# Kernel tuning notes

Measured on AMD Instinct MI355X. Metric: run time of the kernel, lower is better.

The kernel has to match this reference:

```python
import jax, jax.numpy as jnp
import numpy as np
import math

B, S, D, H = 4, 2048, 1024, 16
HD = D // H  # head_dim = 64


def _rope_tables(max_len, half_dim, theta=10000.0):
    inv_freq = 1.0 / (theta ** (jnp.arange(0, half_dim, dtype=jnp.float32) / half_dim))
    ang = jnp.arange(max_len, dtype=jnp.float32)[:, None] * inv_freq[None, :]  # [max_len, half_dim]
    return jnp.cos(ang), jnp.sin(ang)


def _apply_rope(x, cos, sin):
    # x: [B, H, S, HD]; cos/sin: [S, HD/2]
    x1, x2 = x[..., ::2], x[..., 1::2]
    # matches torch.cat([x1*cos - x2*sin, x1*sin + x2*cos], dim=-1)
    return jnp.concatenate([x1 * cos - x2 * sin, x1 * sin + x2 * cos], axis=-1)


def setup_inputs() -> dict:
    key = jax.random.key(0)
    kx, kq, ko = jax.random.split(key, 3)
    x = jax.random.normal(kx, (B, S, D), dtype=jnp.float32)
    Wqkv = jax.random.normal(kq, (D, 3 * D), dtype=jnp.float32) / math.sqrt(D)
    Wout = jax.random.normal(ko, (D, D), dtype=jnp.float32) / math.sqrt(D)
    cos, sin = _rope_tables(S, HD // 2)
    # causal additive mask, per-batch as in module signature [B, S, S]
    causal = jnp.where(jnp.tril(jnp.ones((S, S), dtype=bool)), 0.0, -1e9).astype(jnp.float32)
    mask = jnp.broadcast_to(causal, (B, S, S))
    return {"x": x, "cos": cos, "sin": sin, "mask": mask, "Wqkv": Wqkv, "Wout": Wout}


def reference(x, cos, sin, mask, Wqkv, Wout):
    b, s, d = x.shape
    qkv = x @ Wqkv  # [B, S, 3D]
    q, k, v = jnp.split(qkv, 3, axis=-1)
    def to_heads(t):
        return t.reshape(b, s, H, HD).transpose(0, 2, 1, 3)  # [B, H, S, HD]
    q, k, v = to_heads(q), to_heads(k), to_heads(v)
    q = _apply_rope(q, cos[:s], sin[:s])
    k = _apply_rope(k, cos[:s], sin[:s])
    scores = jnp.einsum("bhqd,bhkd->bhqk", q, k) / math.sqrt(HD)
    attn = jax.nn.softmax(scores + mask[:, None, :, :], axis=-1)
    out = jnp.einsum("bhqk,bhkd->bhqd", attn, v)  # [B, H, S, HD]
    out = out.transpose(0, 2, 1, 3).reshape(b, s, d)
    return out @ Wout
```

## Files before the change

### kernel.cpp

```cpp
#include <hip/hip_runtime.h>
#include <hip/hip_bf16.h>
#include <stdint.h>

#define B_   4
#define S_   2048
#define D_   1024
#define H_   16
#define HD_  64
#define BH_  (B_*H_)
#define MROWS (B_*S_)

typedef short  short8  __attribute__((ext_vector_type(8)));
typedef float  floatx4 __attribute__((ext_vector_type(4)));

__device__ __forceinline__ ushort f2bf(float f) {
    union { float f; uint32_t u; } v; v.f = f;
    uint32_t u = v.u;
    return (ushort)((u + 0x7FFFu + ((u >> 16) & 1u)) >> 16);
}
__device__ __forceinline__ float u2f(uint32_t u) {
    union { uint32_t u; float f; } v; v.u = u; return v.f;
}
__device__ __forceinline__ uint32_t f2u(float f) {
    union { float f; uint32_t u; } v; v.f = f; return v.u;
}

__device__ __forceinline__ void gl_lds16(const ushort* g, ushort* l) {
    __builtin_amdgcn_global_load_lds(
        (const __attribute__((address_space(1))) unsigned int*)g,
        (__attribute__((address_space(3))) unsigned int*)l,
        16, 0, 0);
}

__global__ __launch_bounds__(256)
void k_prep(const float* __restrict__ x, const float* __restrict__ Wqkv,
            const float* __restrict__ Wout,
            ushort* __restrict__ Xbf, ushort* __restrict__ WqkvT, ushort* __restrict__ WoutT) {
    __shared__ float tile[32][33];
    int blk = blockIdx.x;
    int tid = threadIdx.x;
    if (blk >= 4096) {
        int i = (blk - 4096) * 1024 + tid * 4;
        float4 f = *(const float4*)(x + i);
        ushort4 o; o.x = f2bf(f.x); o.y = f2bf(f.y); o.z = f2bf(f.z); o.w = f2bf(f.w);
        *(ushort4*)(Xbf + i) = o;
        return;
    }
    const float* in; ushort* out; int R, C, bx, by;
    if (blk < 3072) { in = Wqkv; out = WqkvT; R = D_; C = 3 * D_; bx = (blk % 96) * 32; by = (blk / 96) * 32; }
    else            { int b2 = blk - 3072; in = Wout; out = WoutT; R = D_; C = D_; bx = (b2 % 32) * 32; by = (b2 / 32) * 32; }
    int tx = tid & 31, ty = tid >> 5;
    #pragma unroll
    for (int j = 0; j < 32; j += 8)
        tile[ty + j][tx] = in[(size_t)(by + ty + j) * C + bx + tx];
    __syncthreads();
    #pragma unroll
    for (int j = 0; j < 32; j += 8)
        out[(size_t)(bx + ty + j) * R + by + tx] = f2bf(tile[tx][ty + j]);
}

#define BM 128
#define BN 128
#define BK 64

template<int EPI>
__global__ __launch_bounds__(256)
void k_gemm(const ushort* __restrict__ A, const ushort* __restrict__ Bt,
            float* __restrict__ outF,
            ushort* __restrict__ q_out, ushort* __restrict__ k_out, ushort* __restrict__ v_out,
            int M, int N, int K) {
    __shared__ __align__(16) ushort As[BM * 64];
    __shared__ __align__(16) ushort Bs[BN * 64];
    int tid  = threadIdx.x;
    int lane = tid & 63;
    int wave = tid >> 6;
    int quad = lane >> 4;
    int l16  = lane & 15;
    int bm = blockIdx.y * BM;
    int bn = blockIdx.x * BN;
    int wm = (wave >> 1) * 64;
    int wn = (wave & 1) * 64;

    floatx4 acc[4][4] = {};

    for (int k0 = 0; k0 < K; k0 += BK) {
        __syncthreads();
        #pragma unroll
        for (int i = 0; i < 4; i++) {
            int c   = i * 256 + tid;
            int row = c >> 3;
            int gc  = (c & 7) ^ (row & 7);
            gl_lds16(&A[(size_t)(bm + row) * K + k0 + gc * 8],  &As[c * 8]);
            gl_lds16(&Bt[(size_t)(bn + row) * K + k0 + gc * 8], &Bs[c * 8]);
        }
        __syncthreads();
        #pragma unroll
        for (int kk = 0; kk < 2; kk++) {
            short8 af[4], bf[4];
            #pragma unroll
            for (int mt = 0; mt < 4; mt++)
                af[mt] = *(const short8*)&As[(wm + mt * 16 + l16) * 64 +
                                             (((kk * 4 + quad) ^ (l16 & 7)) << 3)];
            #pragma unroll
            for (int nt = 0; nt < 4; nt++)
                bf[nt] = *(const short8*)&Bs[(wn + nt * 16 + l16) * 64 +
                                             (((kk * 4 + quad) ^ (l16 & 7)) << 3)];
            #pragma unroll
            for (int mt = 0; mt < 4; mt++)
                #pragma unroll
                for (int nt = 0; nt < 4; nt++)
                    acc[mt][nt] = __builtin_amdgcn_mfma_f32_16x16x32_bf16(af[mt], bf[nt], acc[mt][nt], 0, 0, 0);
        }
    }

    #pragma unroll
    for (int mt = 0; mt < 4; mt++)
        #pragma unroll
        for (int nt = 0; nt < 4; nt++)
            #pragma unroll
            for (int r = 0; r < 4; r++) {
                int row = bm + wm + mt * 16 + quad * 4 + r;
                int col = bn + wn + nt * 16 + l16;
                float v = acc[mt][nt][r];
                if (EPI == 0) {
                    int which = col >> 10;
                    int rem   = col & 1023;
                    int h  = rem >> 6, hd = rem & 63;
                    int b  = row >> 11, s  = row & 2047;
                    size_t idx = ((size_t)(b * H_ + h) * S_ + s) * HD_ + hd;
                    ushort bv = f2bf(v);
                    ushort* dst = (which == 0) ? q_out : (which == 1) ? k_out : v_out;
                    dst[idx] = bv;
                } else {
                    outF[(size_t)row * N + col] = v;
                }
            }
}

__global__ __launch_bounds__(256)
void k_ropevt(ushort* __restrict__ Q, ushort* __restrict__ Kv,
              const ushort* __restrict__ Vb, ushort* __restrict__ VbT,
              const float* __restrict__ cosT, const float* __restrict__ sinT) {
    __shared__ __align__(16) ushort t[64 * 72];
    int blk = blockIdx.x;
    int tid = threadIdx.x;
    if (blk < 32768) {
        int wid  = (blk * 256 + tid) >> 6;
        int lane = tid & 63;
        int s  = wid & (S_ - 1);
        int bh = wid >> 11;
        int i  = lane & 31;
        float c  = cosT[s * 32 + i];
        float sn = sinT[s * 32 + i];
        size_t base = ((size_t)bh * S_ + s) * HD_;

        uint32_t uq = *(const uint32_t*)&Q[base + 2 * i];
        float x1 = u2f(uq << 16), x2 = u2f(uq & 0xFFFF0000u);
        float o  = (lane < 32) ? (x1 * c - x2 * sn) : (x1 * sn + x2 * c);
        Q[base + lane] = f2bf(o * 0.1803368801f);

        uint32_t uk = *(const uint32_t*)&Kv[base + 2 * i];
        x1 = u2f(uk << 16); x2 = u2f(uk & 0xFFFF0000u);
        o  = (lane < 32) ? (x1 * c - x2 * sn) : (x1 * sn + x2 * c);
        Kv[base + lane] = f2bf(o);
        return;
    }
    int b2 = blk - 32768;
    int bh = b2 >> 5;
    int s0 = (b2 & 31) * 64;
    int ss = tid >> 2, c0 = (tid & 3) * 16;
    size_t base = (size_t)bh * S_ * HD_;
    *(uint4*)&t[ss * 72 + c0]     = *(const uint4*)&Vb[base + (size_t)(s0 + ss) * HD_ + c0];
    *(uint4*)&t[ss * 72 + c0 + 8] = *(const uint4*)&Vb[base + (size_t)(s0 + ss) * HD_ + c0 + 8];
    __syncthreads();
    int hd = tid >> 2, q0 = (tid & 3) * 16;
    ushort tmp[16];
    #pragma unroll
    for (int e = 0; e < 16; e++) tmp[e] = t[(q0 + e) * 72 + hd];
    size_t obase = (size_t)bh * HD_ * S_ + (size_t)hd * S_ + s0 + q0;
    *(uint4*)&VbT[obase]     = *(const uint4*)&tmp[0];
    *(uint4*)&VbT[obase + 8] = *(const uint4*)&tmp[8];
}

__global__ __launch_bounds__(256, 4)
void k_attn(const ushort* __restrict__ Q, const ushort* __restrict__ K,
            const ushort* __restrict__ VT, ushort* __restrict__ O) {
    __shared__ __align__(16) ushort Ks[64 * 64];
    __shared__ __align__(16) ushort Vt[64 * 64];
    __shared__ __align__(16) ushort Pst[4][32 * 64];

    const int PI[16] = {15,14,11,10, 12,13,8,9, 2,3,6,7, 1,0,5,4};

    int tid  = threadIdx.x;
    int lane = tid & 63;
    int wave = tid >> 6;
    int quad = lane >> 4;
    int l16  = lane & 15;

    int bh   = blockIdx.x & 63;
    int qblk = PI[blockIdx.x >> 6];
    int qb0  = qblk * 128;
    size_t hbase = (size_t)bh * S_ * HD_;
    size_t vbase = (size_t)bh * HD_ * S_;

    int mrow[2] = { qb0 + wave * 16, qb0 + 64 + wave * 16 };

    short8 qf[2][2];
    #pragma unroll
    for (int m = 0; m < 2; m++)
        #pragma unroll
        for (int h = 0; h < 2; h++)
            qf[m][h] = *(const short8*)&Q[hbase + (size_t)(mrow[m] + l16) * HD_ + quad * 8 + h * 32];

    short8 ones;
    #pragma unroll
    for (int e = 0; e < 8; e++) ones[e] = (short)0x3F80;

    floatx4 acc[2][4] = {};
    floatx4 accl[2] = {};

    int c0r = tid >> 3;
    int c1r = (256 + tid) >> 3;
    const ushort* kp0 = &K[hbase + (size_t)c0r * HD_ + (((tid & 7) ^ (c0r & 7)) << 3)];
    const ushort* kp1 = &K[hbase + (size_t)c1r * HD_ + (((tid & 7) ^ (c1r & 7)) << 3)];
    const ushort* vp0 = &VT[vbase + (size_t)c0r * S_ + (((tid & 7) ^ (c0r & 7)) << 3)];
    const ushort* vp1 = &VT[vbase + (size_t)c1r * S_ + (((tid & 7) ^ (c1r & 7)) << 3)];

    int nk = 2 * qblk + 2;
    for (int kb = 0; kb < nk; kb++) {
        int k0 = kb * 64;
        __syncthreads();
        gl_lds16(kp0, &Ks[tid * 8]);
        gl_lds16(kp1, &Ks[(256 + tid) * 8]);
        gl_lds16(vp0, &Vt[tid * 8]);
        gl_lds16(vp1, &Vt[(256 + tid) * 8]);
        kp0 += 64 * HD_; kp1 += 64 * HD_; vp0 += 64; vp1 += 64;
        __syncthreads();

        bool act[2] = { k0 <= mrow[0] + 15, k0 <= mrow[1] + 15 };

        #pragma unroll
        for (int m = 0; m < 2; m++) {
            if (!act[m]) continue;
            floatx4 sc[4] = {};
            #pragma unroll
            for (int kt = 0; kt < 4; kt++)
                #pragma unroll
                for (int h = 0; h < 2; h++) {
                    short8 kf = *(const short8*)&Ks[(kt * 16 + l16) * 64 +
                                                    (((h * 4 + quad) ^ (l16 & 7)) << 3)];
                    sc[kt] = __builtin_amdgcn_mfma_f32_16x16x32_bf16(kf, qf[m][h], sc[kt], 0, 0, 0);
                }
            bool needMask = (k0 + 63 > mrow[m]);
            int qr = mrow[m] + l16;
            #pragma unroll
            for (int kt = 0; kt < 4; kt++) {
                float p[4];
                #pragma unroll
                for (int r = 0; r < 4; r++) {
                    float v = exp2f(sc[kt][r]);
                    if (needMask) {
                        int kc = k0 + kt * 16 + quad * 4 + r;
                        if (kc > qr) v = 0.0f;
                    }
                    p[r] = v;
                }
                uint2 pk;
                pk.x = __builtin_amdgcn_perm(f2u(p[1]) + 0x8000u, f2u(p[0]) + 0x8000u, 0x07060302u);
                pk.y = __builtin_amdgcn_perm(f2u(p[3]) + 0x8000u, f2u(p[2]) + 0x8000u, 0x07060302u);
                int pc = (kt * 4 + quad) ^ (l16 & 14);
                *(uint2*)&Pst[wave][(m * 16 + l16) * 64 + pc * 4] = pk;
            }
        }

        #pragma unroll
        for (int k2 = 0; k2 < 2; k2++) {
            short8 vb[4];
            #pragma unroll
            for (int nt = 0; nt < 4; nt++)
                vb[nt] = *(const short8*)&Vt[(nt * 16 + l16) * 64 +
                                             (((k2 * 4 + quad) ^ (l16 & 7)) << 3)];
            #pragma unroll
            for (int m = 0; m < 2; m++) {
                if (!act[m]) continue;
                int pe = (k2 * 8 + quad * 2) ^ (l16 & 14);
                short8 pa = *(const short8*)&Pst[wave][(m * 16 + l16) * 64 + pe * 4];
                #pragma unroll
                for (int nt = 0; nt < 4; nt++)
                    acc[m][nt] = __builtin_amdgcn_mfma_f32_16x16x32_bf16(pa, vb[nt], acc[m][nt], 0, 0, 0);
                accl[m] = __builtin_amdgcn_mfma_f32_16x16x32_bf16(pa, ones, accl[m], 0, 0, 0);
            }
        }
    }

    int b = bh >> 4, h = bh & 15;
    #pragma unroll
    for (int m = 0; m < 2; m++)
        #pragma unroll
        for (int r = 0; r < 4; r++) {
            float inv = 1.0f / accl[m][r];
            int qr = mrow[m] + quad * 4 + r;
            #pragma unroll
            for (int nt = 0; nt < 4; nt++)
                O[((size_t)(b * S_ + qr)) * D_ + h * HD_ + nt * 16 + l16] = f2bf(acc[m][nt][r] * inv);
        }
}

extern "C" void kernel_launch(void* const* d_in, const int* in_sizes, int n_in,
                              void* d_out, int out_size, void* d_ws, size_t ws_size,
                              hipStream_t stream) {
    const float* x    = (const float*)d_in[0];
    const float* cosT = (const float*)d_in[1];
    const float* sinT = (const float*)d_in[2];
    const float* Wqkv = (const float*)d_in[4];
    const float* Wout = (const float*)d_in[5];
    float* out = (float*)d_out;

    ushort* ws = (ushort*)d_ws;
    ushort* Xbf    = ws;
    ushort* WqkvT  = Xbf    + (size_t)MROWS * D_;
    ushort* WoutT  = WqkvT  + (size_t)3 * D_ * D_;
    ushort* Qb     = WoutT  + (size_t)D_ * D_;
    ushort* Kb     = Qb     + (size_t)BH_ * S_ * HD_;
    ushort* Vb     = Kb     + (size_t)BH_ * S_ * HD_;
    ushort* VbT    = Vb     + (size_t)BH_ * S_ * HD_;
    ushort* AO     = Xbf;

    k_prep<<<12288, 256, 0, stream>>>(x, Wqkv, Wout, Xbf, WqkvT, WoutT);
    k_gemm<0><<<dim3(3 * D_ / BN, MROWS / BM), 256, 0, stream>>>(Xbf, WqkvT, nullptr, Qb, Kb, Vb,
                                                                 MROWS, 3 * D_, D_);
    k_ropevt<<<34816, 256, 0, stream>>>(Qb, Kb, Vb, VbT, cosT, sinT);
    k_attn<<<1024, 256, 0, stream>>>(Qb, Kb, VbT, AO);
    k_gemm<1><<<dim3(D_ / BN, MROWS / BM), 256, 0, stream>>>(AO, WoutT, out, nullptr, nullptr, nullptr,
                                                             MROWS, D_, D_);
}
```

Baseline: 314.2 us.

## Split attention query block across eight waves and add MFMA priority hints

The attention kernel now runs 512 threads per block, with each of eight waves owning one 16-row query slice instead of four waves each owning two slices. Each thread loads half as much K/V per tile, and the P·V step moves inside the active-row branch. MFMA sections are wrapped in s_setprio, and the bf16 packing of P uses v_cvt_pk_bf16_f32 instead of manual rounding with perm. The intent is more wave-level parallelism and lower register pressure per wave, at the cost of more waves contending at each barrier.

```diff
diff --git a/kernel.cpp b/kernel.cpp
--- a/kernel.cpp
+++ b/kernel.cpp
@@ -182,12 +182,12 @@
     *(uint4*)&VbT[obase + 8] = *(const uint4*)&tmp[8];
 }
 
-__global__ __launch_bounds__(256, 4)
+__global__ __launch_bounds__(512, 8)
 void k_attn(const ushort* __restrict__ Q, const ushort* __restrict__ K,
             const ushort* __restrict__ VT, ushort* __restrict__ O) {
     __shared__ __align__(16) ushort Ks[64 * 64];
     __shared__ __align__(16) ushort Vt[64 * 64];
-    __shared__ __align__(16) ushort Pst[4][32 * 64];
+    __shared__ __align__(16) ushort Pst[8][16 * 64];
 
     const int PI[16] = {15,14,11,10, 12,13,8,9, 2,3,6,7, 1,0,5,4};
 
@@ -203,56 +203,49 @@
     size_t hbase = (size_t)bh * S_ * HD_;
     size_t vbase = (size_t)bh * HD_ * S_;
 
-    int mrow[2] = { qb0 + wave * 16, qb0 + 64 + wave * 16 };
-
-    short8 qf[2][2];
-    #pragma unroll
-    for (int m = 0; m < 2; m++)
-        #pragma unroll
-        for (int h = 0; h < 2; h++)
-            qf[m][h] = *(const short8*)&Q[hbase + (size_t)(mrow[m] + l16) * HD_ + quad * 8 + h * 32];
+    int mrow = qb0 + wave * 16;
+
+    short8 qf[2];
+    #pragma unroll
+    for (int h = 0; h < 2; h++)
+        qf[h] = *(const short8*)&Q[hbase + (size_t)(mrow + l16) * HD_ + quad * 8 + h * 32];
 
     short8 ones;
     #pragma unroll
     for (int e = 0; e < 8; e++) ones[e] = (short)0x3F80;
 
-    floatx4 acc[2][4] = {};
-    floatx4 accl[2] = {};
-
-    int c0r = tid >> 3;
-    int c1r = (256 + tid) >> 3;
-    const ushort* kp0 = &K[hbase + (size_t)c0r * HD_ + (((tid & 7) ^ (c0r & 7)) << 3)];
-    const ushort* kp1 = &K[hbase + (size_t)c1r * HD_ + (((tid & 7) ^ (c1r & 7)) << 3)];
-    const ushort* vp0 = &VT[vbase + (size_t)c0r * S_ + (((tid & 7) ^ (c0r & 7)) << 3)];
-    const ushort* vp1 = &VT[vbase + (size_t)c1r * S_ + (((tid & 7) ^ (c1r & 7)) << 3)];
+    floatx4 acc[4] = {};
+    floatx4 accl = {};
+
+    int srow = tid >> 3;
+    const ushort* kp = &K[hbase + (size_t)srow * HD_ + (((tid & 7) ^ (srow & 7)) << 3)];
+    const ushort* vp = &VT[vbase + (size_t)srow * S_ + (((tid & 7) ^ (srow & 7)) << 3)];
 
     int nk = 2 * qblk + 2;
     for (int kb = 0; kb < nk; kb++) {
         int k0 = kb * 64;
         __syncthreads();
-        gl_lds16(kp0, &Ks[tid * 8]);
-        gl_lds16(kp1, &Ks[(256 + tid) * 8]);
-        gl_lds16(vp0, &Vt[tid * 8]);
-        gl_lds16(vp1, &Vt[(256 + tid) * 8]);
-        kp0 += 64 * HD_; kp1 += 64 * HD_; vp0 += 64; vp1 += 64;
+        gl_lds16(kp, &Ks[tid * 8]);
+        gl_lds16(vp, &Vt[tid * 8]);
+        kp += 64 * HD_; vp += 64;
         __syncthreads();
 
-        bool act[2] = { k0 <= mrow[0] + 15, k0 <= mrow[1] + 15 };
-
-        #pragma unroll
-        for (int m = 0; m < 2; m++) {
-            if (!act[m]) continue;
+        bool act = (k0 <= mrow + 15);
+        if (act) {
             floatx4 sc[4] = {};
+            __builtin_amdgcn_s_setprio(1);
             #pragma unroll
             for (int kt = 0; kt < 4; kt++)
                 #pragma unroll
                 for (int h = 0; h < 2; h++) {
                     short8 kf = *(const short8*)&Ks[(kt * 16 + l16) * 64 +
                                                     (((h * 4 + quad) ^ (l16 & 7)) << 3)];
-                    sc[kt] = __builtin_amdgcn_mfma_f32_16x16x32_bf16(kf, qf[m][h], sc[kt], 0, 0, 0);
+                    sc[kt] = __builtin_amdgcn_mfma_f32_16x16x32_bf16(kf, qf[h], sc[kt], 0, 0, 0);
                 }
-            bool needMask = (k0 + 63 > mrow[m]);
-            int qr = mrow[m] + l16;
+            __builtin_amdgcn_s_setprio(0);
+
+            bool needMask = (k0 + 63 > mrow);
+            int qr = mrow + l16;
             #pragma unroll
             for (int kt = 0; kt < 4; kt++) {
                 float p[4];
@@ -266,44 +259,40 @@
                     p[r] = v;
                 }
                 uint2 pk;
-                pk.x = __builtin_amdgcn_perm(f2u(p[1]) + 0x8000u, f2u(p[0]) + 0x8000u, 0x07060302u);
-                pk.y = __builtin_amdgcn_perm(f2u(p[3]) + 0x8000u, f2u(p[2]) + 0x8000u, 0x07060302u);
+                asm("v_cvt_pk_bf16_f32 %0, %1, %2" : "=v"(pk.x) : "v"(p[0]), "v"(p[1]));
+                asm("v_cvt_pk_bf16_f32 %0, %1, %2" : "=v"(pk.y) : "v"(p[2]), "v"(p[3]));
                 int pc = (kt * 4 + quad) ^ (l16 & 14);
-                *(uint2*)&Pst[wave][(m * 16 + l16) * 64 + pc * 4] = pk;
+                *(uint2*)&Pst[wave][l16 * 64 + pc * 4] = pk;
+            }
+
+            #pragma unroll
+            for (int k2 = 0; k2 < 2; k2++) {
+                short8 vb[4];
+                #pragma unroll
+                for (int nt = 0; nt < 4; nt++)
+                    vb[nt] = *(const short8*)&Vt[(nt * 16 + l16) * 64 +
+                                                 (((k2 * 4 + quad) ^ (l16 & 7)) << 3)];
+                int pe = (k2 * 8 + quad * 2) ^ (l16 & 14);
+                short8 pa = *(const short8*)&Pst[wave][l16 * 64 + pe * 4];
+                __builtin_amdgcn_s_setprio(1);
+                #pragma unroll
+                for (int nt = 0; nt < 4; nt++)
+                    acc[nt] = __builtin_amdgcn_mfma_f32_16x16x32_bf16(pa, vb[nt], acc[nt], 0, 0, 0);
+                accl = __builtin_amdgcn_mfma_f32_16x16x32_bf16(pa, ones, accl, 0, 0, 0);
+                __builtin_amdgcn_s_setprio(0);
             }
         }
-
+    }
+
+    int b = bh >> 4, h = bh & 15;
+    #pragma unroll
+    for (int r = 0; r < 4; r++) {
+        float inv = 1.0f / accl[r];
+        int qr = mrow + quad * 4 + r;
         #pragma unroll
-        for (int k2 = 0; k2 < 2; k2++) {
-            short8 vb[4];
-            #pragma unroll
-            for (int nt = 0; nt < 4; nt++)
-                vb[nt] = *(const short8*)&Vt[(nt * 16 + l16) * 64 +
-                                             (((k2 * 4 + quad) ^ (l16 & 7)) << 3)];
-            #pragma unroll
-            for (int m = 0; m < 2; m++) {
-                if (!act[m]) continue;
-                int pe = (k2 * 8 + quad * 2) ^ (l16 & 14);
-                short8 pa = *(const short8*)&Pst[wave][(m * 16 + l16) * 64 + pe * 4];
-                #pragma unroll
-                for (int nt = 0; nt < 4; nt++)
-                    acc[m][nt] = __builtin_amdgcn_mfma_f32_16x16x32_bf16(pa, vb[nt], acc[m][nt], 0, 0, 0);
-                accl[m] = __builtin_amdgcn_mfma_f32_16x16x32_bf16(pa, ones, accl[m], 0, 0, 0);
-            }
-        }
-    }
-
-    int b = bh >> 4, h = bh & 15;
-    #pragma unroll
-    for (int m = 0; m < 2; m++)
-        #pragma unroll
-        for (int r = 0; r < 4; r++) {
-            float inv = 1.0f / accl[m][r];
-            int qr = mrow[m] + quad * 4 + r;
-            #pragma unroll
-            for (int nt = 0; nt < 4; nt++)
-                O[((size_t)(b * S_ + qr)) * D_ + h * HD_ + nt * 16 + l16] = f2bf(acc[m][nt][r] * inv);
-        }
+        for (int nt = 0; nt < 4; nt++)
+            O[((size_t)(b * S_ + qr)) * D_ + h * HD_ + nt * 16 + l16] = f2bf(acc[nt][r] * inv);
+    }
 }
 
 extern "C" void kernel_launch(void* const* d_in, const int* in_sizes, int n_in,
@@ -330,7 +319,7 @@
     k_gemm<0><<<dim3(3 * D_ / BN, MROWS / BM), 256, 0, stream>>>(Xbf, WqkvT, nullptr, Qb, Kb, Vb,
                                                                  MROWS, 3 * D_, D_);
     k_ropevt<<<34816, 256, 0, stream>>>(Qb, Kb, Vb, VbT, cosT, sinT);
-    k_attn<<<1024, 256, 0, stream>>>(Qb, Kb, VbT, AO);
+    k_attn<<<1024, 512, 0, stream>>>(Qb, Kb, VbT, AO);
     k_gemm<1><<<dim3(D_ / BN, MROWS / BM), 256, 0, stream>>>(AO, WoutT, out, nullptr, nullptr, nullptr,
                                                              MROWS, D_, D_);
 }
```

New measurement: 333.1 us. +6.0%, slower.

## Double-buffer K/V tiles in attention with 512-thread blocks and priority hints

Applied to the files above, without the earlier changes.

Each attention block now has 8 waves covering 256 query rows. K and V tiles are double-buffered in LDS, so the next tile's global-to-LDS load is issued right after a single barrier and overlaps compute on the current tile. The QK^T loop now reuses each K fragment for both row groups, MFMA sections are wrapped in s_setprio, and the bf16 packing uses v_cvt_pk_bf16_f32. In exchange, LDS per block doubles to 64KB, which limits how many blocks fit per CU, and with half as many, longer-running blocks the causal load imbalance across the grid may get worse.

```diff
diff --git a/kernel.cpp b/kernel.cpp
--- a/kernel.cpp
+++ b/kernel.cpp
@@ -182,14 +182,14 @@
     *(uint4*)&VbT[obase + 8] = *(const uint4*)&tmp[8];
 }
 
-__global__ __launch_bounds__(256, 4)
+__global__ __launch_bounds__(512, 4)
 void k_attn(const ushort* __restrict__ Q, const ushort* __restrict__ K,
             const ushort* __restrict__ VT, ushort* __restrict__ O) {
-    __shared__ __align__(16) ushort Ks[64 * 64];
-    __shared__ __align__(16) ushort Vt[64 * 64];
-    __shared__ __align__(16) ushort Pst[4][32 * 64];
-
-    const int PI[16] = {15,14,11,10, 12,13,8,9, 2,3,6,7, 1,0,5,4};
+    __shared__ __align__(16) ushort Ks[2][64 * 64];
+    __shared__ __align__(16) ushort Vt[2][64 * 64];
+    __shared__ __align__(16) ushort Pst[8][32 * 64];
+
+    const int PI[8] = {7,6,5,4, 0,1,2,3};
 
     int tid  = threadIdx.x;
     int lane = tid & 63;
@@ -199,11 +199,11 @@
 
     int bh   = blockIdx.x & 63;
     int qblk = PI[blockIdx.x >> 6];
-    int qb0  = qblk * 128;
+    int qb0  = qblk * 256;
     size_t hbase = (size_t)bh * S_ * HD_;
     size_t vbase = (size_t)bh * HD_ * S_;
 
-    int mrow[2] = { qb0 + wave * 16, qb0 + 64 + wave * 16 };
+    int mrow[2] = { qb0 + wave * 16, qb0 + 128 + wave * 16 };
 
     short8 qf[2][2];
     #pragma unroll
@@ -219,38 +219,53 @@
     floatx4 acc[2][4] = {};
     floatx4 accl[2] = {};
 
-    int c0r = tid >> 3;
-    int c1r = (256 + tid) >> 3;
-    const ushort* kp0 = &K[hbase + (size_t)c0r * HD_ + (((tid & 7) ^ (c0r & 7)) << 3)];
-    const ushort* kp1 = &K[hbase + (size_t)c1r * HD_ + (((tid & 7) ^ (c1r & 7)) << 3)];
-    const ushort* vp0 = &VT[vbase + (size_t)c0r * S_ + (((tid & 7) ^ (c0r & 7)) << 3)];
-    const ushort* vp1 = &VT[vbase + (size_t)c1r * S_ + (((tid & 7) ^ (c1r & 7)) << 3)];
-
-    int nk = 2 * qblk + 2;
+    int srow = tid >> 3;
+    const ushort* kp = &K[hbase + (size_t)srow * HD_ + (((tid & 7) ^ (srow & 7)) << 3)];
+    const ushort* vp = &VT[vbase + (size_t)srow * S_ + (((tid & 7) ^ (srow & 7)) << 3)];
+
+    int nk = 4 * qblk + 4;
+
+    gl_lds16(kp, &Ks[0][tid * 8]);
+    gl_lds16(vp, &Vt[0][tid * 8]);
+
     for (int kb = 0; kb < nk; kb++) {
-        int k0 = kb * 64;
+        int cur = kb & 1;
+        int k0  = kb * 64;
         __syncthreads();
-        gl_lds16(kp0, &Ks[tid * 8]);
-        gl_lds16(kp1, &Ks[(256 + tid) * 8]);
-        gl_lds16(vp0, &Vt[tid * 8]);
-        gl_lds16(vp1, &Vt[(256 + tid) * 8]);
-        kp0 += 64 * HD_; kp1 += 64 * HD_; vp0 += 64; vp1 += 64;
-        __syncthreads();
+        if (kb + 1 < nk) {
+            kp += 64 * HD_; vp += 64;
+            gl_lds16(kp, &Ks[cur ^ 1][tid * 8]);
+            gl_lds16(vp, &Vt[cur ^ 1][tid * 8]);
+        }
 
         bool act[2] = { k0 <= mrow[0] + 15, k0 <= mrow[1] + 15 };
+        if (!act[1]) continue;
+
+        floatx4 sc[2][4];
+        #pragma unroll
+        for (int m = 0; m < 2; m++)
+            if (act[m])
+                #pragma unroll
+                for (int kt = 0; kt < 4; kt++)
+                    sc[m][kt] = (floatx4){0.f, 0.f, 0.f, 0.f};
+
+        __builtin_amdgcn_s_setprio(1);
+        #pragma unroll
+        for (int kt = 0; kt < 4; kt++)
+            #pragma unroll
+            for (int h = 0; h < 2; h++) {
+                short8 kf = *(const short8*)&Ks[cur][(kt * 16 + l16) * 64 +
+                                                     (((h * 4 + quad) ^ (l16 & 7)) << 3)];
+                #pragma unroll
+                for (int m = 0; m < 2; m++)
+                    if (act[m])
+                        sc[m][kt] = __builtin_amdgcn_mfma_f32_16x16x32_bf16(kf, qf[m][h], sc[m][kt], 0, 0, 0);
+            }
+        __builtin_amdgcn_s_setprio(0);
 
         #pragma unroll
         for (int m = 0; m < 2; m++) {
             if (!act[m]) continue;
-            floatx4 sc[4] = {};
-            #pragma unroll
-            for (int kt = 0; kt < 4; kt++)
-                #pragma unroll
-                for (int h = 0; h < 2; h++) {
-                    short8 kf = *(const short8*)&Ks[(kt * 16 + l16) * 64 +
-                                                    (((h * 4 + quad) ^ (l16 & 7)) << 3)];
-                    sc[kt] = __builtin_amdgcn_mfma_f32_16x16x32_bf16(kf, qf[m][h], sc[kt], 0, 0, 0);
-                }
             bool needMask = (k0 + 63 > mrow[m]);
             int qr = mrow[m] + l16;
             #pragma unroll
@@ -258,7 +273,7 @@
                 float p[4];
                 #pragma unroll
                 for (int r = 0; r < 4; r++) {
-                    float v = exp2f(sc[kt][r]);
+                    float v = exp2f(sc[m][kt][r]);
                     if (needMask) {
                         int kc = k0 + kt * 16 + quad * 4 + r;
                         if (kc > qr) v = 0.0f;
@@ -266,8 +281,8 @@
                     p[r] = v;
                 }
                 uint2 pk;
-                pk.x = __builtin_amdgcn_perm(f2u(p[1]) + 0x8000u, f2u(p[0]) + 0x8000u, 0x07060302u);
-                pk.y = __builtin_amdgcn_perm(f2u(p[3]) + 0x8000u, f2u(p[2]) + 0x8000u, 0x07060302u);
+                asm("v_cvt_pk_bf16_f32 %0, %1, %2" : "=v"(pk.x) : "v"(p[0]), "v"(p[1]));
+                asm("v_cvt_pk_bf16_f32 %0, %1, %2" : "=v"(pk.y) : "v"(p[2]), "v"(p[3]));
                 int pc = (kt * 4 + quad) ^ (l16 & 14);
                 *(uint2*)&Pst[wave][(m * 16 + l16) * 64 + pc * 4] = pk;
             }
@@ -278,18 +293,20 @@
             short8 vb[4];
             #pragma unroll
             for (int nt = 0; nt < 4; nt++)
-                vb[nt] = *(const short8*)&Vt[(nt * 16 + l16) * 64 +
-                                             (((k2 * 4 + quad) ^ (l16 & 7)) << 3)];
+                vb[nt] = *(const short8*)&Vt[cur][(nt * 16 + l16) * 64 +
+                                                  (((k2 * 4 + quad) ^ (l16 & 7)) << 3)];
+            int pe = (k2 * 8 + quad * 2) ^ (l16 & 14);
+            __builtin_amdgcn_s_setprio(1);
             #pragma unroll
             for (int m = 0; m < 2; m++) {
                 if (!act[m]) continue;
-                int pe = (k2 * 8 + quad * 2) ^ (l16 & 14);
                 short8 pa = *(const short8*)&Pst[wave][(m * 16 + l16) * 64 + pe * 4];
                 #pragma unroll
                 for (int nt = 0; nt < 4; nt++)
                     acc[m][nt] = __builtin_amdgcn_mfma_f32_16x16x32_bf16(pa, vb[nt], acc[m][nt], 0, 0, 0);
                 accl[m] = __builtin_amdgcn_mfma_f32_16x16x32_bf16(pa, ones, accl[m], 0, 0, 0);
             }
+            __builtin_amdgcn_s_setprio(0);
         }
     }
 
@@ -330,7 +347,7 @@
     k_gemm<0><<<dim3(3 * D_ / BN, MROWS / BM), 256, 0, stream>>>(Xbf, WqkvT, nullptr, Qb, Kb, Vb,
                                                                  MROWS, 3 * D_, D_);
     k_ropevt<<<34816, 256, 0, stream>>>(Qb, Kb, Vb, VbT, cosT, sinT);
-    k_attn<<<1024, 256, 0, stream>>>(Qb, Kb, VbT, AO);
+    k_attn<<<512, 512, 0, stream>>>(Qb, Kb, VbT, AO);
     k_gemm<1><<<dim3(D_ / BN, MROWS / BM), 256, 0, stream>>>(AO, WoutT, out, nullptr, nullptr, nullptr,
                                                              MROWS, D_, D_);
 }
```

After: 382.6 us. +21.8%, slower.
